# Optimization experiments

Measured on AMD Instinct MI355X. Metric: run time of the kernel, lower is better.

Reference implementation:

```python
import jax, jax.numpy as jnp
import numpy as np

N = 100_000      # nodes
E = 3_200_000    # edges (avg degree 32)
F = 16           # irrep feature channels
IR = 4           # (max_l+1)**2 with max_l = 1
DENOM = 32.0     # denominator init kwarg
EPS = 1e-9
INV_S3 = 1.0 / np.sqrt(3.0).astype(np.float32)  # CG norm for 1x1->0
INV_S2 = 1.0 / np.sqrt(2.0).astype(np.float32)  # CG norm for 1x1->1


def setup_inputs() -> dict:
    key = jax.random.key(0)
    k0, k1, k2, k3, k4 = jax.random.split(key, 5)
    positions = jax.random.normal(k0, (N, 3), jnp.float32)
    node_feats = jax.random.normal(k1, (N, F, IR), jnp.float32)
    W = jax.random.normal(k2, (IR, IR), jnp.float32) / np.float32(np.sqrt(IR))
    b = jnp.zeros((IR,), jnp.float32)
    senders = jax.random.randint(k3, (E,), 0, N)
    receivers = jax.random.randint(k4, (E,), 0, N)
    return dict(positions=positions, node_feats=node_feats, W=W, b=b,
                senders=senders, receivers=receivers)


def reference(positions, node_feats, W, b, senders, receivers):
    # --- edge update: SH of normalized relative position, CG tensor product ---
    d = positions[receivers] - positions[senders]               # [E, 3]
    d = d / (jnp.linalg.norm(d, axis=-1, keepdims=True) + EPS)  # unit direction
    # real spherical harmonics up to l=1: sh0 = 1, sh1 = unit direction
    sh1 = d[:, None, :]                                         # [E, 1, 3]

    x = node_feats[senders]                                     # [E, F, 4]
    x0 = x[..., 0:1]                                            # l=0 part [E,F,1]
    x1 = x[..., 1:4]                                            # l=1 part [E,F,3]

    # CG paths with l3 <= max_l = 1:
    #   0x0->0 (identity), 1x1->0 (dot / sqrt3)
    out0 = x0 + jnp.sum(x1 * sh1, axis=-1, keepdims=True) * INV_S3      # [E,F,1]
    #   0x1->1, 1x0->1 (identities), 1x1->1 (cross / sqrt2)
    cross = jnp.cross(x1, jnp.broadcast_to(sh1, x1.shape))
    out1 = x0 * sh1 + x1 + cross * INV_S2                               # [E,F,3]
    tp = jnp.concatenate([out0, out1], axis=-1)                         # [E,F,4]

    # --- node update: segment-sum over receivers, scale, Dense over coeff dim ---
    agg = jax.ops.segment_sum(tp, receivers, num_segments=positions.shape[0])
    agg = agg / DENOM                                                   # [N,F,4]
    return agg @ W + b                                                  # [N,F,4]
```

## Files before the change

kernel.cpp:

```cpp
#include <hip/hip_runtime.h>


#define F_DIM 16
#define BIN_SHIFT 6
#define BIN_NODES (1 << BIN_SHIFT)
#define CHUNK 8192
#define STG (CHUNK / 256)
#define CAP_LDS 2816

__global__ void __launch_bounds__(256) init_kernel(int* __restrict__ binCur,
                                                   int nbins, int cap)
{
    int b = blockIdx.x * blockDim.x + threadIdx.x;
    if (b < nbins) binCur[b] = b * cap;
}

__global__ void __launch_bounds__(256) pos_pack_kernel(
    const float* __restrict__ pos, float4* __restrict__ posf4, int N)
{
    int n = blockIdx.x * blockDim.x + threadIdx.x;
    if (n >= N) return;
    posf4[n] = make_float4(pos[3*n], pos[3*n+1], pos[3*n+2], 0.f);
}

__global__ void __launch_bounds__(256) build_bins_kernel(
    const int* __restrict__ senders, const int* __restrict__ receivers,
    int* __restrict__ binCur, int* __restrict__ bins,
    int nbins, int cap, int E)
{
    __shared__ int hist[2048];
    int t = threadIdx.x;
    for (int i = t; i < nbins; i += 256) hist[i] = 0;
    __syncthreads();

    int base = blockIdx.x * CHUNK;
    unsigned pk[STG], br[STG];
#pragma unroll
    for (int k = 0; k < STG; ++k) {
        int e = base + k * 256 + t;
        if (e < E) {
            int r = receivers[e];
            int s = senders[e];
            int bb = r >> BIN_SHIFT;
            int rank = atomicAdd(&hist[bb], 1);
            pk[k] = ((unsigned)s << BIN_SHIFT) | (unsigned)(r & (BIN_NODES - 1));
            br[k] = ((unsigned)bb << 13) | (unsigned)rank;
        } else {
            br[k] = 0xFFFFFFFFu;
        }
    }
    __syncthreads();

    for (int i = t; i < nbins; i += 256) {
        int c = hist[i];
        if (c > 0) hist[i] = atomicAdd(&binCur[i], c);
    }
    __syncthreads();

#pragma unroll
    for (int k = 0; k < STG; ++k) {
        if (br[k] == 0xFFFFFFFFu) continue;
        int bb   = (int)(br[k] >> 13);
        int rank = (int)(br[k] & 8191u);
        int dest = hist[bb] + rank;
        if (dest < (bb + 1) * cap)
            bins[dest] = (int)pk[k];
    }
}

__device__ __forceinline__ void edge_acc(
    const float4& pr, const float4& sp, const float4& fx,
    float& a0, float& a1, float& a2, float& a3)
{
    const float INV_S3 = 0.5773502691896258f;
    const float INV_S2 = 0.7071067811865476f;
    float dx = pr.x - sp.x;
    float dy = pr.y - sp.y;
    float dz = pr.z - sp.z;
    float d2 = dx*dx + dy*dy + dz*dz;
    float inv = __builtin_amdgcn_rsqf(fmaxf(d2, 1e-18f));
    dx *= inv; dy *= inv; dz *= inv;
    float dot = fx.y*dx + fx.z*dy + fx.w*dz;
    a0 += fx.x + dot * INV_S3;
    float c0 = fx.z*dz - fx.w*dy;
    float c1 = fx.w*dx - fx.y*dz;
    float c2 = fx.y*dy - fx.z*dx;
    a1 += fx.x*dx + fx.y + c0 * INV_S2;
    a2 += fx.x*dy + fx.z + c1 * INV_S2;
    a3 += fx.x*dz + fx.w + c2 * INV_S2;
}

__global__ void __launch_bounds__(256) bin_gather_kernel(
    const float4* __restrict__ posf4,
    const float* __restrict__ nf,
    const int* __restrict__ bins,
    const int* __restrict__ binCur,
    const float* __restrict__ W,
    const float* __restrict__ Bias,
    float* __restrict__ out,
    int N, int cap)
{
    __shared__ int lcsr[CAP_LDS];
    __shared__ int lhist[BIN_NODES];
    __shared__ int lscan[BIN_NODES];
    __shared__ int lstart[BIN_NODES];

    int t = threadIdx.x;
    int bin = blockIdx.x >> 1;
    int fbase = (blockIdx.x & 1) << 3;
    int node0 = bin << BIN_SHIFT;
    int gbase = bin * cap;

    int cnt = binCur[bin] - gbase;
    if (cnt > cap) cnt = cap;

    if (t < BIN_NODES) lhist[t] = 0;
    __syncthreads();

    for (int j = t; j < cnt; j += 256)
        atomicAdd(&lhist[((unsigned)bins[gbase + j]) & (BIN_NODES - 1)], 1);
    __syncthreads();

    if (t < BIN_NODES) lscan[t] = lhist[t];
    __syncthreads();
    for (int off = 1; off < BIN_NODES; off <<= 1) {
        int v = (t < BIN_NODES && t >= off) ? lscan[t - off] : 0;
        __syncthreads();
        if (t < BIN_NODES) lscan[t] += v;
        __syncthreads();
    }
    if (t < BIN_NODES) { lstart[t] = lscan[t] - lhist[t]; lhist[t] = 0; }
    __syncthreads();

    for (int j = t; j < cnt; j += 256) {
        unsigned pk = (unsigned)bins[gbase + j];
        int rl = (int)(pk & (BIN_NODES - 1));
        int rank = atomicAdd(&lhist[rl], 1);
        lcsr[lstart[rl] + rank] = (int)(pk >> BIN_SHIFT);
    }
    __syncthreads();

    float w[16];
#pragma unroll
    for (int i = 0; i < 16; ++i) w[i] = W[i];
    float b0 = Bias[0], b1 = Bias[1], b2 = Bias[2], b3 = Bias[3];
    const float sc = 1.0f / 32.0f;

    int f = fbase + (t & 7);
    const float4* nf4 = (const float4*)nf;

    for (int nl = t >> 3; nl < BIN_NODES; nl += 32) {
        int n = node0 + nl;
        if (n >= N) break;
        float4 pr = posf4[n];
        int s0 = lstart[nl];
        int dcnt = lscan[nl] - s0;

        float a0 = 0.f, a1 = 0.f, a2 = 0.f, a3 = 0.f;
        int j = 0;
        for (; j + 4 <= dcnt; j += 4) {
            int s_0 = lcsr[s0 + j + 0];
            int s_1 = lcsr[s0 + j + 1];
            int s_2 = lcsr[s0 + j + 2];
            int s_3 = lcsr[s0 + j + 3];
            float4 p0 = posf4[s_0];
            float4 p1 = posf4[s_1];
            float4 p2 = posf4[s_2];
            float4 p3 = posf4[s_3];
            float4 q0 = nf4[(unsigned)(s_0 * F_DIM + f)];
            float4 q1 = nf4[(unsigned)(s_1 * F_DIM + f)];
            float4 q2 = nf4[(unsigned)(s_2 * F_DIM + f)];
            float4 q3 = nf4[(unsigned)(s_3 * F_DIM + f)];
            edge_acc(pr, p0, q0, a0, a1, a2, a3);
            edge_acc(pr, p1, q1, a0, a1, a2, a3);
            edge_acc(pr, p2, q2, a0, a1, a2, a3);
            edge_acc(pr, p3, q3, a0, a1, a2, a3);
        }
        for (; j < dcnt; ++j) {
            int s = lcsr[s0 + j];
            float4 p = posf4[s];
            float4 q = nf4[(unsigned)(s * F_DIM + f)];
            edge_acc(pr, p, q, a0, a1, a2, a3);
        }

        a0 *= sc; a1 *= sc; a2 *= sc; a3 *= sc;
        float4 o;
        o.x = a0*w[0] + a1*w[4] + a2*w[8]  + a3*w[12] + b0;
        o.y = a0*w[1] + a1*w[5] + a2*w[9]  + a3*w[13] + b1;
        o.z = a0*w[2] + a1*w[6] + a2*w[10] + a3*w[14] + b2;
        o.w = a0*w[3] + a1*w[7] + a2*w[11] + a3*w[15] + b3;
        ((float4*)out)[(size_t)n * F_DIM + f] = o;
    }
}

__global__ void __launch_bounds__(256) hist_kernel(
    const int* __restrict__ receivers, int* __restrict__ deg,
    int* __restrict__ rank, int E)
{
    int e = blockIdx.x * blockDim.x + threadIdx.x;
    if (e >= E) return;
    rank[e] = atomicAdd(&deg[receivers[e]], 1);
}

__global__ void __launch_bounds__(256) alloc_kernel(
    const int* __restrict__ deg, int* __restrict__ start,
    int* __restrict__ cursor, int N)
{
    __shared__ int tmp[256];
    __shared__ int base;
    int t = threadIdx.x;
    int n = blockIdx.x * blockDim.x + t;
    int v = (n < N) ? deg[n] : 0;
    tmp[t] = v;
    __syncthreads();
    for (int off = 1; off < 256; off <<= 1) {
        int x = (t >= off) ? tmp[t - off] : 0;
        __syncthreads();
        tmp[t] += x;
        __syncthreads();
    }
    int incl = tmp[t];
    if (t == 255) base = atomicAdd(cursor, incl);
    __syncthreads();
    if (n < N) start[n] = base + incl - v;
}

__global__ void __launch_bounds__(256) scatter_kernel(
    const int* __restrict__ senders, const int* __restrict__ receivers,
    const int* __restrict__ rank, const int* __restrict__ start,
    int* __restrict__ csr_s, int E)
{
    int e = blockIdx.x * blockDim.x + threadIdx.x;
    if (e >= E) return;
    csr_s[start[receivers[e]] + rank[e]] = senders[e];
}

__global__ void __launch_bounds__(256) gather_kernel(
    const float* __restrict__ pos,
    const float* __restrict__ nf,
    const int* __restrict__ csr_s,
    const int* __restrict__ start,
    const int* __restrict__ deg,
    const float* __restrict__ W,
    const float* __restrict__ b,
    float* __restrict__ out,
    int N)
{
    const float INV_S3 = 0.5773502691896258f;
    const float INV_S2 = 0.7071067811865476f;

    int tid = blockIdx.x * blockDim.x + threadIdx.x;
    int n = tid >> 4;
    if (n >= N) return;
    int f = tid & 15;

    float rx = pos[3*n], ry = pos[3*n+1], rz = pos[3*n+2];
    int s0 = start[n];
    int dcnt = deg[n];
    float a0 = 0.f, a1 = 0.f, a2 = 0.f, a3 = 0.f;
    const float4* nf4 = (const float4*)nf;

    int s = (dcnt > 0) ? csr_s[s0] : 0;
    for (int j = 0; j < dcnt; ++j) {
        int s_next = (j + 1 < dcnt) ? csr_s[s0 + j + 1] : 0;
        float dx = rx - pos[3*s], dy = ry - pos[3*s+1], dz = rz - pos[3*s+2];
        float d2 = dx*dx + dy*dy + dz*dz;
        float inv = __builtin_amdgcn_rsqf(fmaxf(d2, 1e-18f));
        dx *= inv; dy *= inv; dz *= inv;
        float4 x = nf4[(unsigned)(s * F_DIM + f)];
        float x0 = x.x, x1 = x.y, x2 = x.z, x3 = x.w;
        float dot = x1*dx + x2*dy + x3*dz;
        a0 += x0 + dot * INV_S3;
        float c0 = x2*dz - x3*dy, c1 = x3*dx - x1*dz, c2 = x1*dy - x2*dx;
        a1 += x0*dx + x1 + c0 * INV_S2;
        a2 += x0*dy + x2 + c1 * INV_S2;
        a3 += x0*dz + x3 + c2 * INV_S2;
        s = s_next;
    }
    const float sc = 1.0f / 32.0f;
    a0 *= sc; a1 *= sc; a2 *= sc; a3 *= sc;
    float4 o;
    o.x = a0*W[0] + a1*W[4] + a2*W[8]  + a3*W[12] + b[0];
    o.y = a0*W[1] + a1*W[5] + a2*W[9]  + a3*W[13] + b[1];
    o.z = a0*W[2] + a1*W[6] + a2*W[10] + a3*W[14] + b[2];
    o.w = a0*W[3] + a1*W[7] + a2*W[11] + a3*W[15] + b[3];
    ((float4*)out)[tid] = o;
}

extern "C" void kernel_launch(void* const* d_in, const int* in_sizes, int n_in,
                              void* d_out, int out_size, void* d_ws, size_t ws_size,
                              hipStream_t stream)
{
    const float* pos       = (const float*)d_in[0];
    const float* nf        = (const float*)d_in[1];
    const float* W         = (const float*)d_in[2];
    const float* b         = (const float*)d_in[3];
    const int*   senders   = (const int*)d_in[4];
    const int*   receivers = (const int*)d_in[5];

    int N = in_sizes[0] / 3;
    int E = in_sizes[4];
    float* out = (float*)d_out;
    const int blk = 256;

    int nbins = (N + BIN_NODES - 1) >> BIN_SHIFT;
    int cap   = E / nbins + 453;
    size_t need = ((size_t)N * 4 + (size_t)nbins * cap + nbins) * sizeof(float);

    if (nbins <= 2048 && cap <= CAP_LDS && ws_size >= need) {
        float4* posf4 = (float4*)d_ws;
        int* binCur = (int*)(posf4 + N);
        int* bins   = binCur + nbins;

        pos_pack_kernel<<<(N + blk - 1) / blk, blk, 0, stream>>>(pos, posf4, N);
        init_kernel<<<(nbins + blk - 1) / blk, blk, 0, stream>>>(binCur, nbins, cap);
        build_bins_kernel<<<(E + CHUNK - 1) / CHUNK, blk, 0, stream>>>(
            senders, receivers, binCur, bins, nbins, cap, E);
        bin_gather_kernel<<<nbins * 2, blk, 0, stream>>>(
            posf4, nf, bins, binCur, W, b, out, N, cap);
    } else {
        int* cursor = (int*)d_ws;
        int* deg    = cursor + 1;
        int* start  = deg + N;
        int* rank   = start + N;
        int* csr_s  = rank + E;

        hipMemsetAsync(cursor, 0, (size_t)(1 + N) * sizeof(int), stream);
        hist_kernel<<<(E + blk - 1) / blk, blk, 0, stream>>>(receivers, deg, rank, E);
        alloc_kernel<<<(N + blk - 1) / blk, blk, 0, stream>>>(deg, start, cursor, N);
        scatter_kernel<<<(E + blk - 1) / blk, blk, 0, stream>>>(
            senders, receivers, rank, start, csr_s, E);
        long total = (long)N * F_DIM;
        gather_kernel<<<(unsigned)((total + blk - 1) / blk), blk, 0, stream>>>(
            pos, nf, csr_s, start, deg, W, b, out, N);
    }
}
```

Before: 275.5 us.

## Precompute edge unit directions in LDS and process all features per bin block

Edge direction vectors are computed once per edge while building the per-bin local CSR and stored in shared memory. Each block now handles all 16 feature channels of a bin instead of splitting features across two blocks. Bin size and chunk size are halved so the LDS working set fits. This removes duplicated position gathers, rsqrt work and bin scanning across blocks, at the cost of more LDS per block and a larger build-time histogram.

```diff
diff --git a/kernel.cpp b/kernel.cpp
--- a/kernel.cpp
+++ b/kernel.cpp
@@ -2,11 +2,12 @@
 
 
 #define F_DIM 16
-#define BIN_SHIFT 6
+#define BIN_SHIFT 5
 #define BIN_NODES (1 << BIN_SHIFT)
-#define CHUNK 8192
+#define CHUNK 4096
 #define STG (CHUNK / 256)
-#define CAP_LDS 2816
+#define CAP_LDS 1408
+#define MAXBINS 4096
 
 __global__ void __launch_bounds__(256) init_kernel(int* __restrict__ binCur,
                                                    int nbins, int cap)
@@ -28,7 +29,7 @@
     int* __restrict__ binCur, int* __restrict__ bins,
     int nbins, int cap, int E)
 {
-    __shared__ int hist[2048];
+    __shared__ int hist[MAXBINS];
     int t = threadIdx.x;
     for (int i = t; i < nbins; i += 256) hist[i] = 0;
     __syncthreads();
@@ -68,18 +69,12 @@
     }
 }
 
-__device__ __forceinline__ void edge_acc(
-    const float4& pr, const float4& sp, const float4& fx,
+__device__ __forceinline__ void edge_acc_d(
+    float dx, float dy, float dz, const float4& fx,
     float& a0, float& a1, float& a2, float& a3)
 {
     const float INV_S3 = 0.5773502691896258f;
     const float INV_S2 = 0.7071067811865476f;
-    float dx = pr.x - sp.x;
-    float dy = pr.y - sp.y;
-    float dz = pr.z - sp.z;
-    float d2 = dx*dx + dy*dy + dz*dz;
-    float inv = __builtin_amdgcn_rsqf(fmaxf(d2, 1e-18f));
-    dx *= inv; dy *= inv; dz *= inv;
     float dot = fx.y*dx + fx.z*dy + fx.w*dz;
     a0 += fx.x + dot * INV_S3;
     float c0 = fx.z*dz - fx.w*dy;
@@ -100,14 +95,16 @@
     float* __restrict__ out,
     int N, int cap)
 {
-    __shared__ int lcsr[CAP_LDS];
+    __shared__ int   lcsr[CAP_LDS];
+    __shared__ float ldx[CAP_LDS];
+    __shared__ float ldy[CAP_LDS];
+    __shared__ float ldz[CAP_LDS];
     __shared__ int lhist[BIN_NODES];
     __shared__ int lscan[BIN_NODES];
     __shared__ int lstart[BIN_NODES];
 
     int t = threadIdx.x;
-    int bin = blockIdx.x >> 1;
-    int fbase = (blockIdx.x & 1) << 3;
+    int bin = blockIdx.x;
     int node0 = bin << BIN_SHIFT;
     int gbase = bin * cap;
 
@@ -135,8 +132,20 @@
     for (int j = t; j < cnt; j += 256) {
         unsigned pk = (unsigned)bins[gbase + j];
         int rl = (int)(pk & (BIN_NODES - 1));
+        int s  = (int)(pk >> BIN_SHIFT);
         int rank = atomicAdd(&lhist[rl], 1);
-        lcsr[lstart[rl] + rank] = (int)(pk >> BIN_SHIFT);
+        int dest = lstart[rl] + rank;
+        lcsr[dest] = s;
+        float4 ps = posf4[s];
+        float4 pr = posf4[node0 + rl];
+        float dx = pr.x - ps.x;
+        float dy = pr.y - ps.y;
+        float dz = pr.z - ps.z;
+        float d2 = dx*dx + dy*dy + dz*dz;
+        float inv = __builtin_amdgcn_rsqf(fmaxf(d2, 1e-18f));
+        ldx[dest] = dx * inv;
+        ldy[dest] = dy * inv;
+        ldz[dest] = dz * inv;
     }
     __syncthreads();
 
@@ -146,13 +155,12 @@
     float b0 = Bias[0], b1 = Bias[1], b2 = Bias[2], b3 = Bias[3];
     const float sc = 1.0f / 32.0f;
 
-    int f = fbase + (t & 7);
+    int f = t & 15;
     const float4* nf4 = (const float4*)nf;
 
-    for (int nl = t >> 3; nl < BIN_NODES; nl += 32) {
+    for (int nl = t >> 4; nl < BIN_NODES; nl += 16) {
         int n = node0 + nl;
         if (n >= N) break;
-        float4 pr = posf4[n];
         int s0 = lstart[nl];
         int dcnt = lscan[nl] - s0;
 
@@ -163,24 +171,23 @@
             int s_1 = lcsr[s0 + j + 1];
             int s_2 = lcsr[s0 + j + 2];
             int s_3 = lcsr[s0 + j + 3];
-            float4 p0 = posf4[s_0];
-            float4 p1 = posf4[s_1];
-            float4 p2 = posf4[s_2];
-            float4 p3 = posf4[s_3];
             float4 q0 = nf4[(unsigned)(s_0 * F_DIM + f)];
             float4 q1 = nf4[(unsigned)(s_1 * F_DIM + f)];
             float4 q2 = nf4[(unsigned)(s_2 * F_DIM + f)];
             float4 q3 = nf4[(unsigned)(s_3 * F_DIM + f)];
-            edge_acc(pr, p0, q0, a0, a1, a2, a3);
-            edge_acc(pr, p1, q1, a0, a1, a2, a3);
-            edge_acc(pr, p2, q2, a0, a1, a2, a3);
-            edge_acc(pr, p3, q3, a0, a1, a2, a3);
+            float x0 = ldx[s0 + j + 0], y0 = ldy[s0 + j + 0], z0 = ldz[s0 + j + 0];
+            float x1 = ldx[s0 + j + 1], y1 = ldy[s0 + j + 1], z1 = ldz[s0 + j + 1];
+            float x2 = ldx[s0 + j + 2], y2 = ldy[s0 + j + 2], z2 = ldz[s0 + j + 2];
+            float x3 = ldx[s0 + j + 3], y3 = ldy[s0 + j + 3], z3 = ldz[s0 + j + 3];
+            edge_acc_d(x0, y0, z0, q0, a0, a1, a2, a3);
+            edge_acc_d(x1, y1, z1, q1, a0, a1, a2, a3);
+            edge_acc_d(x2, y2, z2, q2, a0, a1, a2, a3);
+            edge_acc_d(x3, y3, z3, q3, a0, a1, a2, a3);
         }
         for (; j < dcnt; ++j) {
             int s = lcsr[s0 + j];
-            float4 p = posf4[s];
             float4 q = nf4[(unsigned)(s * F_DIM + f)];
-            edge_acc(pr, p, q, a0, a1, a2, a3);
+            edge_acc_d(ldx[s0 + j], ldy[s0 + j], ldz[s0 + j], q, a0, a1, a2, a3);
         }
 
         a0 *= sc; a1 *= sc; a2 *= sc; a3 *= sc;
@@ -304,10 +311,10 @@
     const int blk = 256;
 
     int nbins = (N + BIN_NODES - 1) >> BIN_SHIFT;
-    int cap   = E / nbins + 453;
+    int cap   = E / nbins + 384;
     size_t need = ((size_t)N * 4 + (size_t)nbins * cap + nbins) * sizeof(float);
 
-    if (nbins <= 2048 && cap <= CAP_LDS && ws_size >= need) {
+    if (nbins <= MAXBINS && cap <= CAP_LDS && ws_size >= need) {
         float4* posf4 = (float4*)d_ws;
         int* binCur = (int*)(posf4 + N);
         int* bins   = binCur + nbins;
@@ -316,7 +323,7 @@
         init_kernel<<<(nbins + blk - 1) / blk, blk, 0, stream>>>(binCur, nbins, cap);
         build_bins_kernel<<<(E + CHUNK - 1) / CHUNK, blk, 0, stream>>>(
             senders, receivers, binCur, bins, nbins, cap, E);
-        bin_gather_kernel<<<nbins * 2, blk, 0, stream>>>(
+        bin_gather_kernel<<<nbins, blk, 0, stream>>>(
             posf4, nf, bins, binCur, W, b, out, N, cap);
     } else {
         int* cursor = (int*)d_ws;
```

Result: slower. 287.5 us (+4.4%).
